# Optimization experiments

Measured on AMD Instinct MI355X. Metric: run time of the kernel, lower is better.

## Reference

```python
import jax, jax.numpy as jnp
import numpy as np

B = 128   # batch_size (number of trees / source tweets)
H = 100   # tweet_out_size == GRU hidden == GAT feature dim


def _gru_layer(x, h0, Wih, Whh, bih, bhh):
    # x: [T, N, D] time-major; PyTorch GRU cell math
    def step(h, xt):
        gi = xt @ Wih.T + bih
        gh = h @ Whh.T + bhh
        ir, iz, in_ = jnp.split(gi, 3, axis=-1)
        hr, hz, hn = jnp.split(gh, 3, axis=-1)
        r = jax.nn.sigmoid(ir + hr)
        z = jax.nn.sigmoid(iz + hz)
        n = jnp.tanh(in_ + r * hn)
        h = (1.0 - z) * n + z * h
        return h, h
    hT, ys = jax.lax.scan(step, h0, x)
    return ys, hT


def _gru2(x, h0, Wih0, Whh0, bih0, bhh0, Wih1, Whh1, bih1, bhh1):
    y0, _ = _gru_layer(x, h0[0], Wih0, Whh0, bih0, bhh0)
    _, h1 = _gru_layer(y0, h0[1], Wih1, Whh1, bih1, bhh1)
    return h1  # final hidden of top layer: [N, H]


def _gat(x, ei, W, a_src, a_dst, b, heads, outc, concat):
    # PyG GATConv (eval mode, add_self_loops=True, leaky_relu slope 0.2)
    N = x.shape[0]
    loops = jnp.arange(N, dtype=ei.dtype)
    src = jnp.concatenate([ei[0], loops])
    dst = jnp.concatenate([ei[1], loops])
    h = (x @ W.T).reshape(N, heads, outc)           # [N, H, C]
    es = (h * a_src).sum(-1)                         # [N, H]
    ed = (h * a_dst).sum(-1)
    e = jax.nn.leaky_relu(es[src] + ed[dst], negative_slope=0.2)  # [E, H]
    m = jax.lax.stop_gradient(jax.ops.segment_max(e, dst, num_segments=N))
    ee = jnp.exp(e - m[dst])
    s = jax.ops.segment_sum(ee, dst, num_segments=N)
    alpha = ee / s[dst]
    out = jax.ops.segment_sum(h[src] * alpha[:, :, None], dst, num_segments=N)
    out = out.reshape(N, heads * outc) if concat else out.mean(axis=1)
    return out + b


def _forward(fl, user_text, gnode, gei, tnode, tei, idx):
    (user_feats, h0g, h0t, temb,
     gWih0, gWhh0, gbih0, gbhh0, gWih1, gWhh1, gbih1, gbhh1,
     tWih0, tWhh0, tbih0, tbhh0, tWih1, tWhh1, tbih1, tbhh1,
     uW1, ub1, uW2, ub2,
     gc1W, gc1as, gc1ad, gc1b, gc2W, gc2as, gc2ad, gc2b,
     tc1W, tc1as, tc1ad, tc1b, tc2W, tc2as, tc2ad, tc2b,
     fcW, fcb) = fl
    # --- graphGAT branch ---
    ue = jax.nn.relu(user_feats @ uW1.T + ub1) @ uW2.T + ub2        # [Nu, 100]
    ge = temb[gnode].transpose(1, 0, 2)                              # [T, Ntg, 100]
    hg = _gru2(ge, h0g, gWih0, gWhh0, gbih0, gbhh0, gWih1, gWhh1, gbih1, gbhh1)
    xg = jnp.concatenate([hg[:B], ue, hg[B:]], axis=0)               # [Ng, 100]
    xg = jax.nn.relu(_gat(xg, gei, gc1W, gc1as, gc1ad, gc1b, 8, 64, True))
    xg = jax.nn.relu(_gat(xg, gei, gc2W, gc2as, gc2ad, gc2b, 1, 100, False))
    # --- TreeGAT branch ---
    te = temb[tnode].transpose(1, 0, 2)                              # [T, Ntree, 100]
    ht = _gru2(te, h0t, tWih0, tWhh0, tbih0, tbhh0, tWih1, tWhh1, tbih1, tbhh1)
    xt = ht.at[:B].set(xg[:B])                                       # root rows <- user_root_embed
    xt = jax.nn.relu(_gat(xt, tei, tc1W, tc1as, tc1ad, tc1b, 8, 100, True))
    xt = jax.nn.relu(_gat(xt, tei, tc2W, tc2as, tc2ad, tc2b, 1, 100, False))
    # --- scatter_mean over trees + classifier ---
    ssum = jax.ops.segment_sum(xt, idx, num_segments=B)
    cnt = jax.ops.segment_sum(jnp.ones((xt.shape[0],), xt.dtype), idx, num_segments=B)
    mean = ssum / jnp.maximum(cnt, 1.0)[:, None]
    return mean @ fcW.T + fcb                                        # [B, 4]


def setup_inputs():
    key = jax.random.key(0)
    it = iter(jax.random.split(key, 60))
    def nrm(shape, s):
        return (jax.random.normal(next(it), shape) * s).astype(jnp.float32)
    Ntg, Nu, Ntree = 10000, 20000, 30000
    Ng = Ntg + Nu
    Eg, Et, V, T = 200000, 60000, 50000, 20
    inp = {}
    inp["user_text"] = jax.random.randint(next(it), (Nu, 10), 0, 1000)
    inp["user_feats"] = nrm((Nu, 9), 1.0)
    inp["graph_node_features"] = jax.random.randint(next(it), (Ntg, T), 0, V)
    inp["graph_edge_index"] = jax.random.randint(next(it), (2, Eg), 0, Ng)
    inp["merged_tree_feature"] = jax.random.randint(next(it), (Ntree, T), 0, V)
    inp["merged_tree_edge_index"] = jax.random.randint(next(it), (2, Et), 0, Ntree)
    inp["indices"] = jax.random.randint(next(it), (Ntree,), 0, B)
    inp["h0_graph"] = nrm((2, Ntg, H), 1.0)
    inp["h0_tree"] = nrm((2, Ntree, H), 1.0)
    inp["tweet_emb"] = nrm((V, H), 1.0)
    s = 0.1
    for p in ("g", "t"):
        for l in ("0", "1"):
            inp[p + "Wih" + l] = nrm((3 * H, H), s)
            inp[p + "Whh" + l] = nrm((3 * H, H), s)
            inp[p + "bih" + l] = jnp.zeros((3 * H,), jnp.float32)
            inp[p + "bhh" + l] = jnp.zeros((3 * H,), jnp.float32)
    inp["uW1"] = nrm((100, 9), s);    inp["ub1"] = jnp.zeros((100,), jnp.float32)
    inp["uW2"] = nrm((100, 100), s);  inp["ub2"] = jnp.zeros((100,), jnp.float32)
    inp["gc1W"] = nrm((512, 100), s); inp["gc1as"] = nrm((8, 64), s); inp["gc1ad"] = nrm((8, 64), s); inp["gc1b"] = jnp.zeros((512,), jnp.float32)
    inp["gc2W"] = nrm((100, 512), s); inp["gc2as"] = nrm((1, 100), s); inp["gc2ad"] = nrm((1, 100), s); inp["gc2b"] = jnp.zeros((100,), jnp.float32)
    inp["tc1W"] = nrm((800, 100), s); inp["tc1as"] = nrm((8, 100), s); inp["tc1ad"] = nrm((8, 100), s); inp["tc1b"] = jnp.zeros((800,), jnp.float32)
    inp["tc2W"] = nrm((100, 800), s); inp["tc2as"] = nrm((1, 100), s); inp["tc2ad"] = nrm((1, 100), s); inp["tc2b"] = jnp.zeros((100,), jnp.float32)
    inp["fcW"] = nrm((4, 100), s);    inp["fcb"] = jnp.zeros((4,), jnp.float32)
    return inp


def reference(user_text, user_feats, graph_node_features, graph_edge_index,
              merged_tree_feature, merged_tree_edge_index, indices,
              h0_graph, h0_tree, tweet_emb,
              gWih0, gWhh0, gbih0, gbhh0, gWih1, gWhh1, gbih1, gbhh1,
              tWih0, tWhh0, tbih0, tbhh0, tWih1, tWhh1, tbih1, tbhh1,
              uW1, ub1, uW2, ub2,
              gc1W, gc1as, gc1ad, gc1b, gc2W, gc2as, gc2ad, gc2b,
              tc1W, tc1as, tc1ad, tc1b, tc2W, tc2as, tc2ad, tc2b,
              fcW, fcb):
    fl = (user_feats, h0_graph, h0_tree, tweet_emb,
          gWih0, gWhh0, gbih0, gbhh0, gWih1, gWhh1, gbih1, gbhh1,
          tWih0, tWhh0, tbih0, tbhh0, tWih1, tWhh1, tbih1, tbhh1,
          uW1, ub1, uW2, ub2,
          gc1W, gc1as, gc1ad, gc1b, gc2W, gc2as, gc2ad, gc2b,
          tc1W, tc1as, tc1ad, tc1b, tc2W, tc2as, tc2ad, tc2b,
          fcW, fcb)
    return _forward(fl, user_text, graph_node_features, graph_edge_index,
                    merged_tree_feature, merged_tree_edge_index, indices)
```

## Files before the change

kernel.cpp:

```cpp
#include <hip/hip_runtime.h>

#define NB    128
#define HD    100
#define NU    20000
#define NTG   10000
#define NTREE 30000
#define NG    30000
#define TT    20
#define EG    200000
#define ET    60000
#define VOC   50000

#define ESTR2 448
#define LOG2E  1.4426950408889634f
#define LOG2E2 2.8853900817779268f

typedef unsigned short u16;
typedef unsigned int   u32;
typedef __attribute__((ext_vector_type(8))) short short8;
typedef __attribute__((ext_vector_type(4))) float floatx4;

__device__ __forceinline__ float sigmoid2_(float y) {
    return __fdividef(1.f, 1.f + __builtin_amdgcn_exp2f(-y));
}
__device__ __forceinline__ float tanh2_(float y) {
    return 1.f - __fdividef(2.f, __builtin_amdgcn_exp2f(y) + 1.f);
}
__device__ __forceinline__ u16 f2bf(float f) {
    u32 u = __float_as_uint(f);
    u32 r = (u + 0x7fffu + ((u >> 16) & 1u)) >> 16;
    return (u16)r;
}
__device__ __forceinline__ u16 f2bf_c(float f) {
    u32 r;
    asm("v_cvt_pk_bf16_f32 %0, %1, %2" : "=v"(r) : "v"(f), "v"(f));
    return (u16)r;
}
__device__ __forceinline__ float bf2f(u16 h) {
    return __uint_as_float(((u32)h) << 16);
}

struct GruProb {
    const u16*   Etab;
    const int*   nodes;
    const float* h0;
    const u16*   Whh0;
    const u16*   Wih1;
    const u16*   Whh1;
    u16*         hout;
    int          M;
};

__global__ __launch_bounds__(448, 2) void gru_fused10(GruProb Pg, GruProb Pt, int gblocks)
{
    const bool isg = (int)blockIdx.x < gblocks;
    const GruProb P = isg ? Pg : Pt;
    const int bx = isg ? blockIdx.x : blockIdx.x - gblocks;
    const int M  = P.M;
    const int m0 = bx * 32;

    __shared__ u16 H0[2][32 * 128];
    __shared__ u16 H1[2][32 * 128];
    __shared__ int NID[TT * 32];

    const int tid  = threadIdx.x;
    const int w    = tid >> 6, lane = tid & 63;
    const int fr   = lane & 15, quad = lane >> 4;
    const int c    = w * 16 + fr;
    const bool cok = (c < HD);

    short8 Bh0[3][4], Bx1[3][4], Bh1[3][4];
#pragma unroll
    for (int g = 0; g < 3; ++g) {
        const size_t rb = (size_t)((g * 7 + w) * 16 + fr) * 128 + quad * 8;
#pragma unroll
        for (int kk = 0; kk < 4; ++kk) {
            Bh0[g][kk] = *(const short8*)(P.Whh0 + rb + kk * 32);
            Bx1[g][kk] = *(const short8*)(P.Wih1 + rb + kk * 32);
            Bh1[g][kk] = *(const short8*)(P.Whh1 + rb + kk * 32);
        }
    }

    for (int i = tid; i < 32 * 128; i += 448) {
        H0[0][i] = 0; H0[1][i] = 0; H1[0][i] = 0; H1[1][i] = 0;
    }
    for (int i = tid; i < 32 * TT; i += 448) {
        int row = i / TT, t = i - row * TT;
        int gm = m0 + row;
        NID[t * 32 + row] = (gm < M) ? P.nodes[(size_t)gm * TT + t] : 0;
    }
    __syncthreads();
    if (tid < 32) {
        int off = 200 ^ ((tid & 7) << 4);
        *(u16*)((char*)&H0[0][0] + tid * 256 + off) = 0x3F80;
        *(u16*)((char*)&H0[1][0] + tid * 256 + off) = 0x3F80;
        *(u16*)((char*)&H1[0][0] + tid * 256 + off) = 0x3F80;
        *(u16*)((char*)&H1[1][0] + tid * 256 + off) = 0x3F80;
    }

    float h0f[2][4] = {{0.f,0.f,0.f,0.f},{0.f,0.f,0.f,0.f}};
    float h1f[2][4] = {{0.f,0.f,0.f,0.f},{0.f,0.f,0.f,0.f}};
    if (cok) {
#pragma unroll
        for (int rt = 0; rt < 2; ++rt)
#pragma unroll
        for (int r = 0; r < 4; ++r) {
            int row = rt * 16 + quad * 4 + r;
            int gm  = m0 + row;
            float v0 = 0.f, v1 = 0.f;
            if (gm < M) {
                v0 = P.h0[(size_t)gm * HD + c];
                v1 = P.h0[(size_t)(M + gm) * HD + c];
            }
            h0f[rt][r] = v0; h1f[rt][r] = v1;
            int off = (2 * c) ^ ((row & 7) << 4);
            *(u16*)((char*)&H0[0][0] + row * 256 + off) = f2bf_c(v0);
            *(u16*)((char*)&H1[0][0] + row * 256 + off) = f2bf_c(v1);
        }
    }

    u32 xlo[2][4], xhi[2][4];
    auto xpref = [&](int tn) {
        if (cok) {
#pragma unroll
            for (int rt = 0; rt < 2; ++rt)
#pragma unroll
            for (int r = 0; r < 4; ++r) {
                int row = rt * 16 + quad * 4 + r;
                int nd  = NID[tn * 32 + row];
                uint2 v = *(const uint2*)(P.Etab + (size_t)nd * ESTR2 + c * 4);
                xlo[rt][r] = v.x; xhi[rt][r] = v.y;
            }
        }
    };
    __syncthreads();
    xpref(0);

#pragma unroll
    for (int rt = 0; rt < 2; ++rt) {
        short8 a[4];
#pragma unroll
        for (int kk = 0; kk < 4; ++kk) {
            int row = rt * 16 + fr;
            int off = (kk * 64 + quad * 16) ^ ((row & 7) << 4);
            a[kk] = *(const short8*)((const char*)&H0[0][0] + row * 256 + off);
        }
        floatx4 ag[3];
#pragma unroll
        for (int g = 0; g < 3; ++g) ag[g] = (floatx4){0.f, 0.f, 0.f, 0.f};
#pragma unroll
        for (int g = 0; g < 3; ++g)
#pragma unroll
            for (int kk = 0; kk < 4; ++kk)
                ag[g] = __builtin_amdgcn_mfma_f32_16x16x32_bf16(a[kk], Bh0[g][kk], ag[g], 0, 0, 0);
        if (cok) {
#pragma unroll
            for (int r = 0; r < 4; ++r) {
                int row = rt * 16 + quad * 4 + r;
                float rr = sigmoid2_(bf2f((u16)xlo[rt][r]) + ag[0][r]);
                float zz = sigmoid2_(bf2f((u16)(xlo[rt][r] >> 16)) + ag[1][r]);
                float nn = tanh2_(bf2f((u16)xhi[rt][r]) + rr * ag[2][r]);
                float o  = nn + zz * (h0f[rt][r] - nn);
                h0f[rt][r] = o;
                *(u16*)((char*)&H0[1][0] + row * 256 + ((2 * c) ^ ((row & 7) << 4))) = f2bf_c(o);
            }
        }
    }
    __syncthreads();

    for (int r = 0; r < TT; ++r) {
        const bool doA = (r + 1 < TT);
        if (doA) xpref(r + 1);

        const char* rd0 = (const char*)&H0[(r + 1) & 1][0];
        const char* rd1 = (const char*)&H1[r & 1][0];
        char*       wr0 = (char*)&H0[r & 1][0];
        char*       wr1 = (char*)&H1[(r + 1) & 1][0];

#pragma unroll
        for (int rt = 0; rt < 2; ++rt) {
            short8 a0[4], a1[4];
#pragma unroll
            for (int kk = 0; kk < 4; ++kk) {
                int row = rt * 16 + fr;
                int off = (kk * 64 + quad * 16) ^ ((row & 7) << 4);
                a0[kk] = *(const short8*)(rd0 + row * 256 + off);
                a1[kk] = *(const short8*)(rd1 + row * 256 + off);
            }
            floatx4 rz0 = {0.f,0.f,0.f,0.f}, rz1 = {0.f,0.f,0.f,0.f};
            floatx4 xnv = {0.f,0.f,0.f,0.f}, hnv = {0.f,0.f,0.f,0.f};
#pragma unroll
            for (int kk = 0; kk < 4; ++kk)
                rz0 = __builtin_amdgcn_mfma_f32_16x16x32_bf16(a0[kk], Bx1[0][kk], rz0, 0, 0, 0);
#pragma unroll
            for (int kk = 0; kk < 4; ++kk)
                rz0 = __builtin_amdgcn_mfma_f32_16x16x32_bf16(a1[kk], Bh1[0][kk], rz0, 0, 0, 0);
#pragma unroll
            for (int kk = 0; kk < 4; ++kk)
                rz1 = __builtin_amdgcn_mfma_f32_16x16x32_bf16(a0[kk], Bx1[1][kk], rz1, 0, 0, 0);
#pragma unroll
            for (int kk = 0; kk < 4; ++kk)
                rz1 = __builtin_amdgcn_mfma_f32_16x16x32_bf16(a1[kk], Bh1[1][kk], rz1, 0, 0, 0);
#pragma unroll
            for (int kk = 0; kk < 4; ++kk)
                xnv = __builtin_amdgcn_mfma_f32_16x16x32_bf16(a0[kk], Bx1[2][kk], xnv, 0, 0, 0);
#pragma unroll
            for (int kk = 0; kk < 4; ++kk)
                hnv = __builtin_amdgcn_mfma_f32_16x16x32_bf16(a1[kk], Bh1[2][kk], hnv, 0, 0, 0);
            floatx4 ag[3];
#pragma unroll
            for (int g = 0; g < 3; ++g) ag[g] = (floatx4){0.f, 0.f, 0.f, 0.f};
            if (doA) {
#pragma unroll
                for (int g = 0; g < 3; ++g)
#pragma unroll
                    for (int kk = 0; kk < 4; ++kk)
                        ag[g] = __builtin_amdgcn_mfma_f32_16x16x32_bf16(a0[kk], Bh0[g][kk], ag[g], 0, 0, 0);
            }
            if (cok) {
#pragma unroll
                for (int r4 = 0; r4 < 4; ++r4) {
                    int row = rt * 16 + quad * 4 + r4;
                    float rr = sigmoid2_(rz0[r4]);
                    float zz = sigmoid2_(rz1[r4]);
                    float nn = tanh2_(xnv[r4] + rr * hnv[r4]);
                    float o  = nn + zz * (h1f[rt][r4] - nn);
                    h1f[rt][r4] = o;
                    *(u16*)(wr1 + row * 256 + ((2 * c) ^ ((row & 7) << 4))) = f2bf_c(o);
                }
                if (doA) {
#pragma unroll
                    for (int r4 = 0; r4 < 4; ++r4) {
                        int row = rt * 16 + quad * 4 + r4;
                        float rr = sigmoid2_(bf2f((u16)xlo[rt][r4]) + ag[0][r4]);
                        float zz = sigmoid2_(bf2f((u16)(xlo[rt][r4] >> 16)) + ag[1][r4]);
                        float nn = tanh2_(bf2f((u16)xhi[rt][r4]) + rr * ag[2][r4]);
                        float o  = nn + zz * (h0f[rt][r4] - nn);
                        h0f[rt][r4] = o;
                        *(u16*)(wr0 + row * 256 + ((2 * c) ^ ((row & 7) << 4))) = f2bf_c(o);
                    }
                }
            }
        }
        __syncthreads();
    }

    for (int i = tid; i < 32 * 128; i += 448) {
        int row = i >> 7, cc = i & 127;
        int gm = m0 + row;
        if (gm < M) {
            int off = (2 * cc) ^ ((row & 7) << 4);
            P.hout[(size_t)gm * 128 + cc] = *(const u16*)((const char*)&H1[0][0] + row * 256 + off);
        }
    }
}

#define LDST 40
__global__ __launch_bounds__(256) void gemm_mfma(
    const u16* __restrict__ A, const u16* __restrict__ B,
    float* __restrict__ Cf, u16* __restrict__ Cb,
    int M, int N, int Kt, int lda, int ldw, int ldc)
{
    const int m0 = blockIdx.x * 64;
    if (m0 >= M) return;
    const int n0 = blockIdx.y * 64;

    __shared__ u16 Als[64 * LDST];
    __shared__ u16 Wls[64 * LDST];

    const int tid  = threadIdx.x;
    const int wave = tid >> 6, lane = tid & 63;
    const int row  = tid >> 2, part = (tid & 3) * 8;
    const int fr   = lane & 15, quad = lane >> 4;

    floatx4 acc[4];
#pragma unroll
    for (int t = 0; t < 4; ++t) acc[t] = (floatx4){0.f, 0.f, 0.f, 0.f};

    const int am = m0 + row;  const bool aok = am < M;
    const int wn = n0 + row;  const bool wok = wn < N;
    const uint4 z4 = {0u, 0u, 0u, 0u};

    for (int kk = 0; kk < Kt; ++kk) {
        uint4 av = aok ? *(const uint4*)(A + (size_t)am * lda + kk * 32 + part) : z4;
        uint4 wv = wok ? *(const uint4*)(B + (size_t)wn * ldw + kk * 32 + part) : z4;
        __syncthreads();
        *(uint4*)&Als[row * LDST + part] = av;
        *(uint4*)&Wls[row * LDST + part] = wv;
        __syncthreads();
        short8 af = *(const short8*)&Als[((wave << 4) + fr) * LDST + quad * 8];
#pragma unroll
        for (int t = 0; t < 4; ++t) {
            short8 bf = *(const short8*)&Wls[((t << 4) + fr) * LDST + quad * 8];
            acc[t] = __builtin_amdgcn_mfma_f32_16x16x32_bf16(af, bf, acc[t], 0, 0, 0);
        }
    }

    const int orow0 = m0 + (wave << 4) + quad * 4;
#pragma unroll
    for (int t = 0; t < 4; ++t) {
        int col = n0 + (t << 4) + fr;
        if (col >= N) continue;
#pragma unroll
        for (int r = 0; r < 4; ++r) {
            int mr = orow0 + r;
            if (mr >= M) continue;
            float v = acc[t][r];
            if (Cf) Cf[(size_t)mr * ldc + col] = v;
            if (Cb) Cb[(size_t)mr * ldc + col] = f2bf(v);
        }
    }
}

__global__ __launch_bounds__(256) void gemm_etab(
    const u16* __restrict__ A, const u16* __restrict__ W0, const u16* __restrict__ W1,
    u16* __restrict__ C0, u16* __restrict__ C1)
{
    const int m0 = blockIdx.x * 64;
    const int n0 = blockIdx.y * 64;
    const u16* B = blockIdx.z ? W1 : W0;
    u16* Cb = blockIdx.z ? C1 : C0;
    const int N = 400;

    __shared__ u16 Als[64 * LDST];
    __shared__ u16 Wls[64 * LDST];

    const int tid  = threadIdx.x;
    const int wave = tid >> 6, lane = tid & 63;
    const int row  = tid >> 2, part = (tid & 3) * 8;
    const int fr   = lane & 15, quad = lane >> 4;

    floatx4 acc[4];
#pragma unroll
    for (int t = 0; t < 4; ++t) acc[t] = (floatx4){0.f, 0.f, 0.f, 0.f};

    const int am = m0 + row;
    const int wn = n0 + row;  const bool wok = wn < N;
    const uint4 z4 = {0u, 0u, 0u, 0u};

    for (int kk = 0; kk < 4; ++kk) {
        uint4 av = *(const uint4*)(A + (size_t)am * 128 + kk * 32 + part);
        uint4 wv = wok ? *(const uint4*)(B + (size_t)wn * 128 + kk * 32 + part) : z4;
        __syncthreads();
        *(uint4*)&Als[row * LDST + part] = av;
        *(uint4*)&Wls[row * LDST + part] = wv;
        __syncthreads();
        short8 af = *(const short8*)&Als[((wave << 4) + fr) * LDST + quad * 8];
#pragma unroll
        for (int t = 0; t < 4; ++t) {
            short8 bf = *(const short8*)&Wls[((t << 4) + fr) * LDST + quad * 8];
            acc[t] = __builtin_amdgcn_mfma_f32_16x16x32_bf16(af, bf, acc[t], 0, 0, 0);
        }
    }

    const int orow0 = m0 + (wave << 4) + quad * 4;
#pragma unroll
    for (int t = 0; t < 4; ++t) {
        int col = n0 + (t << 4) + fr;
        if (col >= N) continue;
#pragma unroll
        for (int r = 0; r < 4; ++r)
            Cb[(size_t)(orow0 + r) * ESTR2 + col] = f2bf(acc[t][r]);
    }
}

__global__ __launch_bounds__(256) void gemm_nt(
    const float* __restrict__ A, const float* __restrict__ W,
    const float* __restrict__ bias, float* __restrict__ C,
    int M, int N, int K, int relu)
{
    const int m0 = blockIdx.x * 64;
    const int n0 = blockIdx.y * 64;
    __shared__ float As[20][68];
    __shared__ float Ws[20][68];
    const int tid = threadIdx.x;
    const int r0 = (tid >> 4) * 4;
    const int c0 = (tid & 15) * 4;
    int sr[5], sk[5];
#pragma unroll
    for (int it = 0; it < 5; ++it) {
        int idx = tid + it * 256;
        sr[it] = idx / 20; sk[it] = idx - sr[it] * 20;
    }
    float acc[4][4];
#pragma unroll
    for (int i = 0; i < 4; ++i)
#pragma unroll
        for (int j = 0; j < 4; ++j) acc[i][j] = 0.f;
    const int nch = (K + 19) / 20;
    for (int ch = 0; ch < nch; ++ch) {
        const int k0 = ch * 20;
#pragma unroll
        for (int it = 0; it < 5; ++it) {
            int m = m0 + sr[it], k = k0 + sk[it];
            float va = 0.f, vw = 0.f;
            if (k < K) {
                if (m < M) va = A[(size_t)m * K + k];
                int n = n0 + sr[it];
                if (n < N) vw = W[(size_t)n * K + k];
            }
            As[sk[it]][sr[it]] = va;
            Ws[sk[it]][sr[it]] = vw;
        }
        __syncthreads();
#pragma unroll
        for (int kkk = 0; kkk < 20; ++kkk) {
            float4 a = *(const float4*)&As[kkk][r0];
            float4 w = *(const float4*)&Ws[kkk][c0];
            float av[4] = {a.x, a.y, a.z, a.w};
            float wv[4] = {w.x, w.y, w.z, w.w};
#pragma unroll
            for (int i = 0; i < 4; ++i)
#pragma unroll
                for (int j = 0; j < 4; ++j)
                    acc[i][j] = fmaf(av[i], wv[j], acc[i][j]);
        }
        __syncthreads();
    }
#pragma unroll
    for (int i = 0; i < 4; ++i) {
        int m = m0 + r0 + i;
        if (m >= M) continue;
#pragma unroll
        for (int j = 0; j < 4; ++j) {
            int n = n0 + c0 + j;
            if (n >= N) continue;
            float v = acc[i][j] + (bias ? bias[n] : 0.f);
            if (relu) v = fmaxf(v, 0.f);
            C[(size_t)m * N + n] = v;
        }
    }
}

struct CvtAll {
    const float* temb;  u16* tembB;
    const float* gsrc[6]; const float* gbias[6]; u16* gdst[6];
    const float* is[2];   const float* ib[2];    u16* id_[2];
    const float* wsrc[4]; u16* wdst[4];
    int wK[4]; int wLdk[4]; int wTot[4];
};
#define CB_TEMB 25000
#define CB_GRUW 168
#define CB_IH0  224
#define CB_WTOT 1169

__global__ void convert_all(CvtAll P)
{
    int b = blockIdx.x;
    const int tid = threadIdx.x;
    if (b < CB_TEMB) {
        int t = b * 256 + tid;
        int n = t >> 7, c = t & 127;
        u16 o = 0;
        if (c < 100) o = f2bf(P.temb[(size_t)n * 100 + c]);
        else if (c == 100) o = 0x3F80;
        P.tembB[t] = o;
        return;
    }
    b -= CB_TEMB;
    if (b < 6 * CB_GRUW) {
        int mat = b / CB_GRUW;
        int t = (b - mat * CB_GRUW) * 256 + tid;
        int rr = t >> 7, cc = t & 127;
        int g = rr / 112, r2 = rr - g * 112;
        u16 o = 0;
        if (r2 < 100) {
            float sc = (g == 2) ? LOG2E2 : LOG2E;
            int sr = g * 100 + r2;
            if (cc < 100) o = f2bf(P.gsrc[mat][(size_t)sr * 100 + cc] * sc);
            else if (cc == 100) o = f2bf(P.gbias[mat][sr] * sc);
        }
        P.gdst[mat][t] = o;
        return;
    }
    b -= 6 * CB_GRUW;
    if (b < 2 * CB_IH0) {
        int which = b / CB_IH0;
        int t = (b - which * CB_IH0) * 256 + tid;
        int j = t >> 7, kc = t & 127;
        int cc = j >> 2, g = j & 3;
        u16 o = 0;
        if (g < 3 && cc < 100) {
            float sc = (g == 2) ? LOG2E2 : LOG2E;
            int sr = g * 100 + cc;
            if (kc < 100) o = f2bf(P.is[which][(size_t)sr * 100 + kc] * sc);
            else if (kc == 100) o = f2bf(P.ib[which][sr] * sc);
        }
        P.id_[which][t] = o;
        return;
    }
    b -= 2 * CB_IH0;
    int seg, t;
    if (b < 256)      { seg = 0; t = b * 256 + tid; }
    else if (b < 456) { seg = 1; t = (b - 256) * 256 + tid; }
    else if (b < 856) { seg = 2; t = (b - 456) * 256 + tid; }
    else              { seg = 3; t = (b - 856) * 256 + tid; }
    if (t >= P.wTot[seg]) return;
    int K = P.wK[seg], ldk = P.wLdk[seg];
    int n = t / ldk, c = t - n * ldk;
    u16 o = (c < K) ? f2bf(P.wsrc[seg][(size_t)n * K + c]) : (u16)0;
    P.wdst[seg][t] = o;
}

__global__ void build_xg_bf(const u16* __restrict__ hgb, const float* __restrict__ ue,
                            u16* __restrict__ xgb)
{
    int t = blockIdx.x * blockDim.x + threadIdx.x;
    if (t >= NG * 128) return;
    int n = t >> 7, c = t & 127;
    u16 o = 0;
    if (n < NB)           o = hgb[n * 128 + c];
    else if (n < NB + NU) { if (c < HD) o = f2bf(ue[(size_t)(n - NB) * HD + c]); }
    else                  o = hgb[(size_t)(n - NU) * 128 + c];
    xgb[t] = o;
}

__global__ void set_roots(const float* __restrict__ src, u16* __restrict__ hb)
{
    int t = blockIdx.x * blockDim.x + threadIdx.x;
    if (t >= NB * HD) return;
    int n = t / HD, c = t - n * HD;
    hb[(size_t)n * 128 + c] = f2bf(src[t]);
}

__global__ void csr_count2(const int* __restrict__ gei, const int* __restrict__ tei,
                           const int* __restrict__ bmap,
                           int* __restrict__ gcnt, int* __restrict__ tcnt,
                           int* __restrict__ bcnt)
{
    int e = blockIdx.x * blockDim.x + threadIdx.x;
    const int GE = EG + NG, TE = ET + NTREE;
    if (e < GE) {
        int dst = (e < EG) ? gei[EG + e] : e - EG;
        atomicAdd(&gcnt[dst], 1);
    } else if (e < GE + TE) {
        int e2 = e - GE;
        int dst = (e2 < ET) ? tei[ET + e2] : e2 - ET;
        atomicAdd(&tcnt[dst], 1);
    } else {
        int e3 = e - GE - TE;
        if (e3 >= NTREE) return;
        atomicAdd(&bcnt[bmap[e3]], 1);
    }
}

__global__ void csr_scan2(int* __restrict__ gcnt, int* __restrict__ goff, int* __restrict__ gcur,
                          int* __restrict__ tcnt, int* __restrict__ toff, int* __restrict__ tcur,
                          int* __restrict__ bcnt, int* __restrict__ boff, int* __restrict__ bcur)
{
    const int* cnt; int* off; int* cur; int N;
    if (blockIdx.x == 0)      { cnt = gcnt; off = goff; cur = gcur; N = NG; }
    else if (blockIdx.x == 1) { cnt = tcnt; off = toff; cur = tcur; N = NTREE; }
    else                      { cnt = bcnt; off = boff; cur = bcur; N = NB; }
    __shared__ int part[256];
    const int tid = threadIdx.x;
    const int per = (N + 255) / 256;
    const int i0 = tid * per;
    const int i1 = min(i0 + per, N);
    int s = 0;
    for (int i = i0; i < i1; ++i) s += cnt[i];
    part[tid] = s;
    __syncthreads();
    for (int o = 1; o < 256; o <<= 1) {
        int u = (tid >= o) ? part[tid - o] : 0;
        __syncthreads();
        part[tid] += u;
        __syncthreads();
    }
    int base = part[tid] - s;
    for (int i = i0; i < i1; ++i) {
        off[i] = base; cur[i] = base;
        base += cnt[i];
    }
    if (tid == 255) off[N] = part[255];
}

__global__ void csr_scatter2(const int* __restrict__ gei, const int* __restrict__ tei,
                             const int* __restrict__ bmap,
                             int* __restrict__ gcur, int* __restrict__ tcur,
                             int* __restrict__ bcur,
                             int* __restrict__ geidx, int* __restrict__ teidx,
                             int* __restrict__ bidx)
{
    int e = blockIdx.x * blockDim.x + threadIdx.x;
    const int GE = EG + NG, TE = ET + NTREE;
    if (e < GE) {
        int dst = (e < EG) ? gei[EG + e] : e - EG;
        int pos = atomicAdd(&gcur[dst], 1);
        geidx[pos] = e;
    } else if (e < GE + TE) {
        int e2 = e - GE;
        int dst = (e2 < ET) ? tei[ET + e2] : e2 - ET;
        int pos = atomicAdd(&tcur[dst], 1);
        teidx[pos] = e2;
    } else {
        int e3 = e - GE - TE;
        if (e3 >= NTREE) return;
        int pos = atomicAdd(&bcur[bmap[e3]], 1);
        bidx[pos] = e3;
    }
}

__global__ void gat_es_ed(const u16* __restrict__ feat, const float* __restrict__ asrc,
                          const float* __restrict__ adst, float* __restrict__ es,
                          float* __restrict__ ed, int N, int heads, int C)
{
    int gid = blockIdx.x * blockDim.x + threadIdx.x;
    if (gid >= N * heads) return;
    int n = gid / heads, hd = gid - n * heads;
    const u16* hp = feat + ((size_t)n * heads + hd) * C;
    const float* as = asrc + (size_t)hd * C;
    const float* ad = adst + (size_t)hd * C;
    float s1 = 0.f, s2 = 0.f;
    for (int c = 0; c < C; c += 4) {
        uint2 pk = *(const uint2*)(hp + c);
        float v0 = bf2f((u16)(pk.x & 0xffff)), v1 = bf2f((u16)(pk.x >> 16));
        float v2 = bf2f((u16)(pk.y & 0xffff)), v3 = bf2f((u16)(pk.y >> 16));
        s1 += v0 * as[c] + v1 * as[c + 1] + v2 * as[c + 2] + v3 * as[c + 3];
        s2 += v0 * ad[c] + v1 * ad[c + 1] + v2 * ad[c + 2] + v3 * ad[c + 3];
    }
    es[gid] = s1; ed[gid] = s2;
}

template<int C, int VEC, int HEADS, int NCHUNK>
__global__ __launch_bounds__(256) void gat_fused(
    const int* __restrict__ off, const int* __restrict__ eidx,
    const int* __restrict__ ei, int E,
    const float* __restrict__ es, const float* __restrict__ ed,
    const u16* __restrict__ feat, const float* __restrict__ bias,
    float* __restrict__ outf, u16* __restrict__ outb,
    int N, int HC)
{
    int gt = blockIdx.x * blockDim.x + threadIdx.x;
    int wid = gt >> 6, lane = gt & 63;
    int dst = wid / NCHUNK, chunk = wid - dst * NCHUNK;
    if (dst >= N) return;
    const int e0 = off[dst], e1 = off[dst + 1];

    const int hd  = lane & (HEADS - 1);
    const int esl = lane / HEADS;
    const int EPI = 64 / HEADS;
    float edv = ed[(size_t)dst * HEADS + hd];

    float mymax = -3.4e38f;
    for (int p = e0 + esl; p < e1; p += EPI) {
        int j = eidx[p];
        int src = (j < E) ? ei[j] : (j - E);
        float e = es[(size_t)src * HEADS + hd] + edv;
        e = e > 0.f ? e : 0.2f * e;
        mymax = fmaxf(mymax, e);
    }
#pragma unroll
    for (int o = HEADS; o < 64; o <<= 1)
        mymax = fmaxf(mymax, __shfl_xor(mymax, o));

    float ssum = 0.f;
    for (int p = e0 + esl; p < e1; p += EPI) {
        int j = eidx[p];
        int src = (j < E) ? ei[j] : (j - E);
        float e = es[(size_t)src * HEADS + hd] + edv;
        e = e > 0.f ? e : 0.2f * e;
        ssum += __expf(e - mymax);
    }
#pragma unroll
    for (int o = HEADS; o < 64; o <<= 1)
        ssum += __shfl_xor(ssum, o);
    float sinv = __fdividef(1.f, ssum);

    int c0 = chunk * 64 * VEC + lane * VEC;
    int split = (c0 / C + 1) * C - c0;
    int hlo = c0 / C;              if (hlo > HEADS - 1) hlo = HEADS - 1;
    int hhi = (c0 + VEC - 1) / C;  if (hhi > HEADS - 1) hhi = HEADS - 1;
    float maxlo = __shfl(mymax, hlo), sinvlo = __shfl(sinv, hlo), edlo = __shfl(edv, hlo);
    float maxhi = __shfl(mymax, hhi), sinvhi = __shfl(sinv, hhi), edhi = __shfl(edv, hhi);

    if (c0 >= HC) return;
    float acc[VEC];
#pragma unroll
    for (int v = 0; v < VEC; ++v) acc[v] = 0.f;

    for (int p = e0; p < e1; ++p) {
        int j = eidx[p];
        int src = (j < E) ? ei[j] : (j - E);
        float elo = es[(size_t)src * HEADS + hlo] + edlo;
        elo = elo > 0.f ? elo : 0.2f * elo;
        float alo = __expf(elo - maxlo) * sinvlo;
        float ahi = alo;
        if (hhi != hlo) {
            float ehi = es[(size_t)src * HEADS + hhi] + edhi;
            ehi = ehi > 0.f ? ehi : 0.2f * ehi;
            ahi = __expf(ehi - maxhi) * sinvhi;
        }
        const u16* frp = feat + (size_t)src * HC + c0;
        float fv[VEC];
        if (VEC == 8) {
            uint4 pk = *(const uint4*)frp;
            fv[0] = bf2f((u16)(pk.x & 0xffff)); fv[1] = bf2f((u16)(pk.x >> 16));
            fv[2] = bf2f((u16)(pk.y & 0xffff)); fv[3] = bf2f((u16)(pk.y >> 16));
            fv[4] = bf2f((u16)(pk.z & 0xffff)); fv[5] = bf2f((u16)(pk.z >> 16));
            fv[6] = bf2f((u16)(pk.w & 0xffff)); fv[7] = bf2f((u16)(pk.w >> 16));
        } else {
            u32 pk = *(const u32*)frp;
            fv[0] = bf2f((u16)(pk & 0xffff)); fv[1] = bf2f((u16)(pk >> 16));
        }
#pragma unroll
        for (int v = 0; v < VEC; ++v) {
            float a = (v < split) ? alo : ahi;
            acc[v] += fv[v] * a;
        }
    }
#pragma unroll
    for (int v = 0; v < VEC; ++v) {
        int c = c0 + v;
        if (c >= HC) continue;
        float o = fmaxf(acc[v] + bias[c], 0.f);
        if (outf) outf[(size_t)dst * HC + c] = o;
        if (outb) outb[(size_t)dst * HC + c] = f2bf(o);
    }
}

__global__ void scatter_mean_csr(const int* __restrict__ boff, const int* __restrict__ bidx,
                                 const float* __restrict__ x, float* __restrict__ meanb)
{
    int b = blockIdx.x;
    int tid = threadIdx.x;
    int c = tid & 127, half = tid >> 7;
    __shared__ float partial[256];
    int i0 = boff[b], i1 = boff[b + 1];
    float acc = 0.f;
    if (c < HD) {
        for (int i = i0 + half; i < i1; i += 2)
            acc += x[(size_t)bidx[i] * HD + c];
    }
    partial[tid] = acc;
    __syncthreads();
    if (half == 0 && c < HD) {
        float tot = partial[tid] + partial[tid + 128];
        float cnt = (float)(i1 - i0);
        meanb[b * HD + c] = tot * __fdividef(1.f, fmaxf(cnt, 1.f));
    }
}

__global__ void fc_out2(const float* __restrict__ meanb, const float* __restrict__ W,
                        const float* __restrict__ b, float* __restrict__ out)
{
    int t = threadIdx.x;
    int bb = t >> 2, j = t & 3;
    float acc = b[j];
    for (int k = 0; k < HD; ++k) acc += meanb[bb * HD + k] * W[j * HD + k];
    out[t] = acc;
}

extern "C" void kernel_launch(void* const* d_in, const int* in_sizes, int n_in,
                              void* d_out, int out_size, void* d_ws, size_t ws_size,
                              hipStream_t stream)
{
    const float* user_feats = (const float*)d_in[1];
    const int*   gnf        = (const int*)d_in[2];
    const int*   gei        = (const int*)d_in[3];
    const int*   tnf        = (const int*)d_in[4];
    const int*   tei        = (const int*)d_in[5];
    const int*   indices    = (const int*)d_in[6];
    const float* h0g        = (const float*)d_in[7];
    const float* h0t        = (const float*)d_in[8];
    const float* temb       = (const float*)d_in[9];
    const float* gW[2][4] = {{(const float*)d_in[10], (const float*)d_in[11], (const float*)d_in[12], (const float*)d_in[13]},
                             {(const float*)d_in[14], (const float*)d_in[15], (const float*)d_in[16], (const float*)d_in[17]}};
    const float* tW[2][4] = {{(const float*)d_in[18], (const float*)d_in[19], (const float*)d_in[20], (const float*)d_in[21]},
                             {(const float*)d_in[22], (const float*)d_in[23], (const float*)d_in[24], (const float*)d_in[25]}};
    const float* uW1 = (const float*)d_in[26]; const float* ub1 = (const float*)d_in[27];
    const float* uW2 = (const float*)d_in[28]; const float* ub2 = (const float*)d_in[29];
    const float* gc1W = (const float*)d_in[30]; const float* gc1as = (const float*)d_in[31];
    const float* gc1ad = (const float*)d_in[32]; const float* gc1b = (const float*)d_in[33];
    const float* gc2W = (const float*)d_in[34]; const float* gc2as = (const float*)d_in[35];
    const float* gc2ad = (const float*)d_in[36]; const float* gc2b = (const float*)d_in[37];
    const float* tc1W = (const float*)d_in[38]; const float* tc1as = (const float*)d_in[39];
    const float* tc1ad = (const float*)d_in[40]; const float* tc1b = (const float*)d_in[41];
    const float* tc2W = (const float*)d_in[42]; const float* tc2as = (const float*)d_in[43];
    const float* tc2ad = (const float*)d_in[44]; const float* tc2b = (const float*)d_in[45];
    const float* fcW = (const float*)d_in[46]; const float* fcb = (const float*)d_in[47];
    float* out = (float*)d_out;

    char* ws = (char*)d_ws;
    const size_t NEED = 226500000;
    if (ws_size < NEED) return;

    float* XGF    = (float*)(ws + 0);
    u16*   TEMB_B = (u16*)(ws + 12000000);
    u16*   ETAB_G = (u16*)(ws + 25000000);
    u16*   ETAB_T = (u16*)(ws + 70000000);
    u16*   GH1B   = (u16*)(ws + 115000000);
    u16*   TH1B   = (u16*)(ws + 117600000);
    float* UE     = (float*)(ws + 125300000);
    float* HID    = (float*)(ws + 133400000);
    u16*   WARENA = (u16*)(ws + 141500000);
    int*   GOFF   = (int*)(ws + 142700000);
    int*   GCUR   = (int*)(ws + 142900000);
    int*   GCNT   = (int*)(ws + 143100000);
    int*   TCNT   = (int*)(ws + 143220000);
    int*   BCNT   = (int*)(ws + 143340000);
    int*   GEIDX  = (int*)(ws + 143400000);
    int*   TOFF   = (int*)(ws + 144400000);
    int*   TCUR   = (int*)(ws + 144600000);
    int*   TEIDX  = (int*)(ws + 144800000);
    int*   BOFF   = (int*)(ws + 145160000);
    int*   BCUR   = (int*)(ws + 145170000);
    int*   BIDX   = (int*)(ws + 145180000);
    float* ESB    = (float*)(ws + 145300000);
    float* EDB    = (float*)(ws + 146300000);
    float* MEANB  = (float*)(ws + 156700000);
    u16*   XG_B   = (u16*)(ws + 157000000);
    u16*   GFEAT1 = (u16*)(ws + 165000000);
    u16*   W_G1a  = (u16*)(ws + 196000000);
    u16*   W_G2a  = (u16*)(ws + 196131072);
    u16*   W_G1b  = (u16*)(ws + 196233472);
    u16*   W_G2b  = (u16*)(ws + 196438272);
    u16*   GOUT1B = (u16*)(ws + 25000000);
    u16*   GFEAT2 = (u16*)(ws + 56000000);
    u16*   TFEAT1 = (u16*)(ws + 25000000);
    u16*   TOUT1B = (u16*)(ws + 74000000);
    u16*   TFEAT2 = (u16*)(ws + 123000000);
    float* XOUT2  = (float*)(ws + 157000000);

    u16* gWHH0  = WARENA + 0;
    u16* gWIH1  = WARENA + 43008;
    u16* gWHH1  = WARENA + 86016;
    u16* tWHH0  = WARENA + 129024;
    u16* tWIH1  = WARENA + 172032;
    u16* tWHH1  = WARENA + 215040;
    u16* W_IH0A = WARENA + 258048;
    u16* W_IH0B = WARENA + 315392;

    auto mfma = [&](const u16* A, int lda, const u16* W, int ldw,
                    float* Cf, u16* Cb, int ldc, int M, int N, int Kt) {
        dim3 grid((M + 63) / 64, (N + 63) / 64, 1);
        gemm_mfma<<<grid, 256, 0, stream>>>(A, W, Cf, Cb, M, N, Kt, lda, ldw, ldc);
    };

    {
        CvtAll P;
        P.temb = temb; P.tembB = TEMB_B;
        P.gsrc[0] = gW[0][1]; P.gbias[0] = gW[0][3]; P.gdst[0] = gWHH0;
        P.gsrc[1] = gW[1][0]; P.gbias[1] = gW[1][2]; P.gdst[1] = gWIH1;
        P.gsrc[2] = gW[1][1]; P.gbias[2] = gW[1][3]; P.gdst[2] = gWHH1;
        P.gsrc[3] = tW[0][1]; P.gbias[3] = tW[0][3]; P.gdst[3] = tWHH0;
        P.gsrc[4] = tW[1][0]; P.gbias[4] = tW[1][2]; P.gdst[4] = tWIH1;
        P.gsrc[5] = tW[1][1]; P.gbias[5] = tW[1][3]; P.gdst[5] = tWHH1;
        P.is[0] = gW[0][0]; P.ib[0] = gW[0][2]; P.id_[0] = W_IH0A;
        P.is[1] = tW[0][0]; P.ib[1] = tW[0][2]; P.id_[1] = W_IH0B;
        P.wsrc[0] = gc1W; P.wdst[0] = W_G1a; P.wK[0] = 100; P.wLdk[0] = 128; P.wTot[0] = 512 * 128;
        P.wsrc[1] = gc2W; P.wdst[1] = W_G2a; P.wK[1] = 512; P.wLdk[1] = 512; P.wTot[1] = 100 * 512;
        P.wsrc[2] = tc1W; P.wdst[2] = W_G1b; P.wK[2] = 100; P.wLdk[2] = 128; P.wTot[2] = 800 * 128;
        P.wsrc[3] = tc2W; P.wdst[3] = W_G2b; P.wK[3] = 800; P.wLdk[3] = 800; P.wTot[3] = 100 * 800;
        int grid = CB_TEMB + 6 * CB_GRUW + 2 * CB_IH0 + CB_WTOT;
        convert_all<<<grid, 256, 0, stream>>>(P);
    }

    {
        dim3 ge((VOC + 63) / 64, 7, 2);
        gemm_etab<<<ge, 256, 0, stream>>>(TEMB_B, W_IH0A, W_IH0B, ETAB_G, ETAB_T);
    }

    hipMemsetAsync(GCNT, 0, 240512, stream);
    {
        int tot = (EG + NG) + (ET + NTREE) + NTREE;
        csr_count2<<<(tot + 255) / 256, 256, 0, stream>>>(gei, tei, indices, GCNT, TCNT, BCNT);
        csr_scan2<<<3, 256, 0, stream>>>(GCNT, GOFF, GCUR, TCNT, TOFF, TCUR, BCNT, BOFF, BCUR);
        csr_scatter2<<<(tot + 255) / 256, 256, 0, stream>>>(gei, tei, indices,
                                                            GCUR, TCUR, BCUR, GEIDX, TEIDX, BIDX);
    }

    {
        dim3 g1((NU + 63) / 64, (HD + 63) / 64, 1);
        gemm_nt<<<g1, 256, 0, stream>>>(user_feats, uW1, ub1, HID, NU, HD, 9, 1);
        gemm_nt<<<g1, 256, 0, stream>>>(HID, uW2, ub2, UE, NU, HD, HD, 0);
    }

    {
        GruProb Pg = { ETAB_G, gnf, h0g, gWHH0, gWIH1, gWHH1, GH1B, NTG };
        GruProb Pt = { ETAB_T, tnf, h0t, tWHH0, tWIH1, tWHH1, TH1B, NTREE };
        int gblk = (NTG + 31) / 32;
        int tblk = (NTREE + 31) / 32;
        gru_fused10<<<gblk + tblk, 448, 0, stream>>>(Pg, Pt, gblk);
    }

    build_xg_bf<<<(NG * 128 + 255) / 256, 256, 0, stream>>>(GH1B, UE, XG_B);
    {
        mfma(XG_B, 128, W_G1a, 128, nullptr, GFEAT1, 512, NG, 512, 4);
        gat_es_ed<<<(NG * 8 + 255) / 256, 256, 0, stream>>>(GFEAT1, gc1as, gc1ad, ESB, EDB, NG, 8, 64);
        gat_fused<64, 8, 8, 1><<<(NG + 3) / 4, 256, 0, stream>>>(
            GOFF, GEIDX, gei, EG, ESB, EDB, GFEAT1, gc1b, nullptr, GOUT1B, NG, 512);
    }
    {
        mfma(GOUT1B, 512, W_G2a, 512, nullptr, GFEAT2, 100, NG, 100, 16);
        gat_es_ed<<<(NG + 255) / 256, 256, 0, stream>>>(GFEAT2, gc2as, gc2ad, ESB, EDB, NG, 1, 100);
        gat_fused<100, 2, 1, 1><<<(NG + 3) / 4, 256, 0, stream>>>(
            GOFF, GEIDX, gei, EG, ESB, EDB, GFEAT2, gc2b, XGF, nullptr, NG, 100);
    }

    set_roots<<<(NB * HD + 255) / 256, 256, 0, stream>>>(XGF, TH1B);
    {
        mfma(TH1B, 128, W_G1b, 128, nullptr, TFEAT1, 800, NTREE, 800, 4);
        gat_es_ed<<<(NTREE * 8 + 255) / 256, 256, 0, stream>>>(TFEAT1, tc1as, tc1ad, ESB, EDB, NTREE, 8, 100);
        gat_fused<100, 8, 8, 2><<<(NTREE * 2 + 3) / 4, 256, 0, stream>>>(
            TOFF, TEIDX, tei, ET, ESB, EDB, TFEAT1, tc1b, nullptr, TOUT1B, NTREE, 800);
    }
    {
        mfma(TOUT1B, 800, W_G2b, 800, nullptr, TFEAT2, 100, NTREE, 100, 25);
        gat_es_ed<<<(NTREE + 255) / 256, 256, 0, stream>>>(TFEAT2, tc2as, tc2ad, ESB, EDB, NTREE, 1, 100);
        gat_fused<100, 2, 1, 1><<<(NTREE + 3) / 4, 256, 0, stream>>>(
            TOFF, TEIDX, tei, ET, ESB, EDB, TFEAT2, tc2b, XOUT2, nullptr, NTREE, 100);
    }

    scatter_mean_csr<<<NB, 256, 0, stream>>>(BOFF, BIDX, XOUT2, MEANB);
    fc_out2<<<1, 512, 0, stream>>>(MEANB, fcW, fcb, out);
}
```

Before: 1.440 ms.

## Fuse GAT attention-score reductions into MFMA GEMM epilogue and simplify first MLP layer

The GAT source and destination attention dot products are now computed in the gemm_mfma epilogue from the fp32 accumulators, using lane shuffles and atomicAdd into per-layer es/ed buffers, which removes four separate gat_es_ed launches and their re-reads of the bf16 features. The es/ed buffers are now distinct per layer and zeroed by a larger memset that also covers the CSR counters. Separately, the K=9 first user-MLP layer moves from a tiled GEMM to a simple elementwise dot-product kernel. In exchange, the change adds atomic traffic, a much larger memset, and reductions that now use unrounded fp32 values rather than the stored bf16 features.

```diff
diff --git a/kernel.cpp b/kernel.cpp
--- a/kernel.cpp
+++ b/kernel.cpp
@@ -259,7 +259,9 @@
 __global__ __launch_bounds__(256) void gemm_mfma(
     const u16* __restrict__ A, const u16* __restrict__ B,
     float* __restrict__ Cf, u16* __restrict__ Cb,
-    int M, int N, int Kt, int lda, int ldw, int ldc)
+    int M, int N, int Kt, int lda, int ldw, int ldc,
+    const float* __restrict__ asrc, const float* __restrict__ adst,
+    float* __restrict__ es, float* __restrict__ ed, int heads, int Cc)
 {
     const int m0 = blockIdx.x * 64;
     if (m0 >= M) return;
@@ -308,6 +310,53 @@
             float v = acc[t][r];
             if (Cf) Cf[(size_t)mr * ldc + col] = v;
             if (Cb) Cb[(size_t)mr * ldc + col] = f2bf(v);
+        }
+    }
+
+    if (es) {
+        const int hA = n0 / Cc;
+        int hB = (n0 + 63) / Cc; if (hB > heads - 1) hB = heads - 1;
+        float pse[2][4], psd[2][4];
+#pragma unroll
+        for (int s = 0; s < 2; ++s)
+#pragma unroll
+        for (int r = 0; r < 4; ++r) { pse[s][r] = 0.f; psd[s][r] = 0.f; }
+#pragma unroll
+        for (int t = 0; t < 4; ++t) {
+            int col = n0 + (t << 4) + fr;
+            if (col >= N) continue;
+            int h = col / Cc;
+            int slot = (h != hA);
+            float as = asrc[h * Cc + (col - h * Cc)];
+            float ad = adst[h * Cc + (col - h * Cc)];
+#pragma unroll
+            for (int r = 0; r < 4; ++r) {
+                pse[slot][r] += acc[t][r] * as;
+                psd[slot][r] += acc[t][r] * ad;
+            }
+        }
+#pragma unroll
+        for (int o = 1; o < 16; o <<= 1) {
+#pragma unroll
+            for (int s = 0; s < 2; ++s)
+#pragma unroll
+            for (int r = 0; r < 4; ++r) {
+                pse[s][r] += __shfl_xor(pse[s][r], o);
+                psd[s][r] += __shfl_xor(psd[s][r], o);
+            }
+        }
+        if (fr == 0) {
+#pragma unroll
+            for (int r = 0; r < 4; ++r) {
+                int mr = orow0 + r;
+                if (mr >= M) continue;
+                atomicAdd(&es[(size_t)mr * heads + hA], pse[0][r]);
+                atomicAdd(&ed[(size_t)mr * heads + hA], psd[0][r]);
+                if (hB != hA) {
+                    atomicAdd(&es[(size_t)mr * heads + hB], pse[1][r]);
+                    atomicAdd(&ed[(size_t)mr * heads + hB], psd[1][r]);
+                }
+            }
         }
     }
 }
@@ -430,6 +479,20 @@
             C[(size_t)m * N + n] = v;
         }
     }
+}
+
+__global__ void mlp1(const float* __restrict__ uf, const float* __restrict__ W,
+                     const float* __restrict__ b, float* __restrict__ out)
+{
+    int t = blockIdx.x * blockDim.x + threadIdx.x;
+    if (t >= NU * HD) return;
+    int n = t / HD, j = t - n * HD;
+    const float* ur = uf + (size_t)n * 9;
+    const float* wr = W + (size_t)j * 9;
+    float acc = b[j];
+#pragma unroll
+    for (int k = 0; k < 9; ++k) acc = fmaf(ur[k], wr[k], acc);
+    out[t] = fmaxf(acc, 0.f);
 }
 
 struct CvtAll {
@@ -599,27 +662,6 @@
         int pos = atomicAdd(&bcur[bmap[e3]], 1);
         bidx[pos] = e3;
     }
-}
-
-__global__ void gat_es_ed(const u16* __restrict__ feat, const float* __restrict__ asrc,
-                          const float* __restrict__ adst, float* __restrict__ es,
-                          float* __restrict__ ed, int N, int heads, int C)
-{
-    int gid = blockIdx.x * blockDim.x + threadIdx.x;
-    if (gid >= N * heads) return;
-    int n = gid / heads, hd = gid - n * heads;
-    const u16* hp = feat + ((size_t)n * heads + hd) * C;
-    const float* as = asrc + (size_t)hd * C;
-    const float* ad = adst + (size_t)hd * C;
-    float s1 = 0.f, s2 = 0.f;
-    for (int c = 0; c < C; c += 4) {
-        uint2 pk = *(const uint2*)(hp + c);
-        float v0 = bf2f((u16)(pk.x & 0xffff)), v1 = bf2f((u16)(pk.x >> 16));
-        float v2 = bf2f((u16)(pk.y & 0xffff)), v3 = bf2f((u16)(pk.y >> 16));
-        s1 += v0 * as[c] + v1 * as[c + 1] + v2 * as[c + 2] + v3 * as[c + 3];
-        s2 += v0 * ad[c] + v1 * ad[c + 1] + v2 * ad[c + 2] + v3 * ad[c + 3];
-    }
-    es[gid] = s1; ed[gid] = s2;
 }
 
 template<int C, int VEC, int HEADS, int NCHUNK>
@@ -806,8 +848,14 @@
     int*   BOFF   = (int*)(ws + 145160000);
     int*   BCUR   = (int*)(ws + 145170000);
     int*   BIDX   = (int*)(ws + 145180000);
-    float* ESB    = (float*)(ws + 145300000);
-    float* EDB    = (float*)(ws + 146300000);
+    float* ES1    = (float*)(ws + 145300000);
+    float* ED1    = (float*)(ws + 146300000);
+    float* ES2    = (float*)(ws + 147300000);
+    float* ED2    = (float*)(ws + 147450000);
+    float* ES3    = (float*)(ws + 147600000);
+    float* ED3    = (float*)(ws + 148600000);
+    float* ES4    = (float*)(ws + 149600000);
+    float* ED4    = (float*)(ws + 149750000);
     float* MEANB  = (float*)(ws + 156700000);
     u16*   XG_B   = (u16*)(ws + 157000000);
     u16*   GFEAT1 = (u16*)(ws + 165000000);
@@ -832,9 +880,13 @@
     u16* W_IH0B = WARENA + 315392;
 
     auto mfma = [&](const u16* A, int lda, const u16* W, int ldw,
-                    float* Cf, u16* Cb, int ldc, int M, int N, int Kt) {
+                    float* Cf, u16* Cb, int ldc, int M, int N, int Kt,
+                    const float* as = nullptr, const float* ad = nullptr,
+                    float* es = nullptr, float* ed = nullptr,
+                    int heads = 1, int Cc = 1) {
         dim3 grid((M + 63) / 64, (N + 63) / 64, 1);
-        gemm_mfma<<<grid, 256, 0, stream>>>(A, W, Cf, Cb, M, N, Kt, lda, ldw, ldc);
+        gemm_mfma<<<grid, 256, 0, stream>>>(A, W, Cf, Cb, M, N, Kt, lda, ldw, ldc,
+                                            as, ad, es, ed, heads, Cc);
     };
 
     {
@@ -861,7 +913,7 @@
         gemm_etab<<<ge, 256, 0, stream>>>(TEMB_B, W_IH0A, W_IH0B, ETAB_G, ETAB_T);
     }
 
-    hipMemsetAsync(GCNT, 0, 240512, stream);
+    hipMemsetAsync(GOFF, 0, 149870000 - 142700000, stream);
     {
         int tot = (EG + NG) + (ET + NTREE) + NTREE;
         csr_count2<<<(tot + 255) / 256, 256, 0, stream>>>(gei, tei, indices, GCNT, TCNT, BCNT);
@@ -870,9 +922,9 @@
                                                             GCUR, TCUR, BCUR, GEIDX, TEIDX, BIDX);
     }
 
+    mlp1<<<(NU * HD + 255) / 256, 256, 0, stream>>>(user_feats, uW1, ub1, HID);
     {
         dim3 g1((NU + 63) / 64, (HD + 63) / 64, 1);
-        gemm_nt<<<g1, 256, 0, stream>>>(user_feats, uW1, ub1, HID, NU, HD, 9, 1);
         gemm_nt<<<g1, 256, 0, stream>>>(HID, uW2, ub2, UE, NU, HD, HD, 0);
     }
 
@@ -886,30 +938,30 @@
 
     build_xg_bf<<<(NG * 128 + 255) / 256, 256, 0, stream>>>(GH1B, UE, XG_B);
     {
-        mfma(XG_B, 128, W_G1a, 128, nullptr, GFEAT1, 512, NG, 512, 4);
-        gat_es_ed<<<(NG * 8 + 255) / 256, 256, 0, stream>>>(GFEAT1, gc1as, gc1ad, ESB, EDB, NG, 8, 64);
+        mfma(XG_B, 128, W_G1a, 128, nullptr, GFEAT1, 512, NG, 512, 4,
+             gc1as, gc1ad, ES1, ED1, 8, 64);
         gat_fused<64, 8, 8, 1><<<(NG + 3) / 4, 256, 0, stream>>>(
-            GOFF, GEIDX, gei, EG, ESB, EDB, GFEAT1, gc1b, nullptr, GOUT1B, NG, 512);
+            GOFF, GEIDX, gei, EG, ES1, ED1, GFEAT1, gc1b, nullptr, GOUT1B, NG, 512);
     }
     {
-        mfma(GOUT1B, 512, W_G2a, 512, nullptr, GFEAT2, 100, NG, 100, 16);
-        gat_es_ed<<<(NG + 255) / 256, 256, 0, stream>>>(GFEAT2, gc2as, gc2ad, ESB, EDB, NG, 1, 100);
+        mfma(GOUT1B, 512, W_G2a, 512, nullptr, GFEAT2, 100, NG, 100, 16,
+             gc2as, gc2ad, ES2, ED2, 1, 100);
         gat_fused<100, 2, 1, 1><<<(NG + 3) / 4, 256, 0, stream>>>(
-            GOFF, GEIDX, gei, EG, ESB, EDB, GFEAT2, gc2b, XGF, nullptr, NG, 100);
+            GOFF, GEIDX, gei, EG, ES2, ED2, GFEAT2, gc2b, XGF, nullptr, NG, 100);
     }
 
     set_roots<<<(NB * HD + 255) / 256, 256, 0, stream>>>(XGF, TH1B);
     {
-        mfma(TH1B, 128, W_G1b, 128, nullptr, TFEAT1, 800, NTREE, 800, 4);
-        gat_es_ed<<<(NTREE * 8 + 255) / 256, 256, 0, stream>>>(TFEAT1, tc1as, tc1ad, ESB, EDB, NTREE, 8, 100);
+        mfma(TH1B, 128, W_G1b, 128, nullptr, TFEAT1, 800, NTREE, 800, 4,
+             tc1as, tc1ad, ES3, ED3, 8, 100);
         gat_fused<100, 8, 8, 2><<<(NTREE * 2 + 3) / 4, 256, 0, stream>>>(
-            TOFF, TEIDX, tei, ET, ESB, EDB, TFEAT1, tc1b, nullptr, TOUT1B, NTREE, 800);
+            TOFF, TEIDX, tei, ET, ES3, ED3, TFEAT1, tc1b, nullptr, TOUT1B, NTREE, 800);
     }
     {
-        mfma(TOUT1B, 800, W_G2b, 800, nullptr, TFEAT2, 100, NTREE, 100, 25);
-        gat_es_ed<<<(NTREE + 255) / 256, 256, 0, stream>>>(TFEAT2, tc2as, tc2ad, ESB, EDB, NTREE, 1, 100);
+        mfma(TOUT1B, 800, W_G2b, 800, nullptr, TFEAT2, 100, NTREE, 100, 25,
+             tc2as, tc2ad, ES4, ED4, 1, 100);
         gat_fused<100, 2, 1, 1><<<(NTREE + 3) / 4, 256, 0, stream>>>(
-            TOFF, TEIDX, tei, ET, ESB, EDB, TFEAT2, tc2b, XOUT2, nullptr, NTREE, 100);
+            TOFF, TEIDX, tei, ET, ES4, ED4, TFEAT2, tc2b, XOUT2, nullptr, NTREE, 100);
     }
 
     scatter_mean_csr<<<NB, 256, 0, stream>>>(BOFF, BIDX, XOUT2, MEANB);
```

Result: no change. 1.424 ms (-1.2%).
